# Optimization experiments

Hardware: AMD Instinct MI355X
Metric: run time of the kernel (lower is better)

Reference implementation:

```python
import jax, jax.numpy as jnp
import numpy as np

THETA = 10000.0

def apply_rope(x, positions):
    # x: [B, H, S, d_k], positions: [S] int
    d_k = x.shape[-1]
    inv_freq = THETA ** (-jnp.arange(0, d_k, 2, dtype=jnp.float32) / d_k)  # [d_k/2]
    ang = positions.astype(jnp.float32)[:, None] * inv_freq[None, :]        # [S, d_k/2]
    cos, sin = jnp.cos(ang), jnp.sin(ang)
    x_even = x[..., 0::2]
    x_odd = x[..., 1::2]
    r_even = x_even * cos - x_odd * sin
    r_odd = x_even * sin + x_odd * cos
    # interleave back
    return jnp.stack([r_even, r_odd], axis=-1).reshape(x.shape)

def setup_inputs() -> dict:
    key = jax.random.key(0)
    k1, k2, k3 = jax.random.split(key, 3)
    B, S, D = 2, 2048, 1024
    x = jax.random.normal(k1, (B, S, D), dtype=jnp.float32)
    token_positions = jnp.arange(S, dtype=jnp.int32)
    W_qkv = jax.random.normal(k2, (3 * D, D), dtype=jnp.float32) * 0.02
    W_o = jax.random.normal(k3, (D, D), dtype=jnp.float32) * 0.02
    return {"x": x, "token_positions": token_positions, "W_qkv": W_qkv, "W_o": W_o}

def reference(x, token_positions, W_qkv, W_o):
    B, S, D = x.shape
    H = 16
    d_k = D // H
    qkv = jnp.einsum('bsd,ed->bse', x, W_qkv)           # [B, S, 3D]
    q, k, v = jnp.split(qkv, 3, axis=-1)
    def to_heads(t):
        return t.reshape(B, S, H, d_k).transpose(0, 2, 1, 3)  # [B, H, S, d_k]
    hq, hk, hv = to_heads(q), to_heads(k), to_heads(v)
    hq = apply_rope(hq, token_positions)
    hk = apply_rope(hk, token_positions)
    scale = d_k ** -0.5
    scores = jnp.einsum('bhqd,bhkd->bhqk', hq, hk) * scale  # [B, H, S, S]
    causal = jnp.tril(jnp.ones((S, S), dtype=bool))
    scores = jnp.where(causal, scores, -jnp.inf)
    attn = jax.nn.softmax(scores, axis=-1)
    out = jnp.einsum('bhqk,bhkd->bhqd', attn, hv)           # [B, H, S, d_k]
    out = out.transpose(0, 2, 1, 3).reshape(B, S, D)
    return jnp.einsum('bsd,ed->bse', out, W_o)
```

## Files before the change

### kernel.cpp

```cpp
#include <hip/hip_runtime.h>
#include <math.h>

typedef short short8 __attribute__((ext_vector_type(8)));
typedef float f32x4 __attribute__((ext_vector_type(4)));

typedef __attribute__((address_space(1))) const void* as1p;
typedef __attribute__((address_space(3))) void* as3p;

__device__ __forceinline__ unsigned short f2bf(float f) {
    unsigned int u = __float_as_uint(f);
    u += 0x7fffu + ((u >> 16) & 1u);
    return (unsigned short)(u >> 16);
}
__device__ __forceinline__ float bf2f(unsigned int bits) {
    return __uint_as_float(bits << 16);
}

__global__ void cvt_all_bf16(const float* __restrict__ x,
                             const float* __restrict__ wqkv,
                             const float* __restrict__ wo,
                             unsigned short* __restrict__ xb,
                             unsigned short* __restrict__ wqkvb,
                             unsigned short* __restrict__ wob) {
    int i = blockIdx.x * blockDim.x + threadIdx.x;
    const float* src;
    unsigned short* dst;
    int off;
    if (i < 1048576)       { src = x;    dst = xb;    off = i; }
    else if (i < 1835008)  { src = wqkv; dst = wqkvb; off = i - 1048576; }
    else                   { src = wo;   dst = wob;   off = i - 1835008; }
    float4 v = ((const float4*)src)[off];
    ushort4 o = make_ushort4(f2bf(v.x), f2bf(v.y), f2bf(v.z), f2bf(v.w));
    ((ushort4*)dst)[off] = o;
}

template <int RF, int NTX, bool BF16_OUT, bool DO_ROPE>
__global__ __launch_bounds__(256) void gemm_nt_mfma(
    const unsigned short* __restrict__ A, const unsigned short* __restrict__ B,
    void* __restrict__ Cv, const int* __restrict__ pos, int N, int K) {
    constexpr int BM = RF * 32;
    __shared__ unsigned short As[BM * 32];
    __shared__ unsigned short Bs[128 * 32];
    const int tid = threadIdx.x;
    const int wave = tid >> 6, lane = tid & 63;
    const int L = blockIdx.x;
    const int xcd = L & 7, idx = L >> 3;
    const int nt_ = xcd * NTX + idx % NTX;
    const int mt  = idx / NTX;
    const int m0 = mt * BM, n0 = nt_ << 7;
    const int wr = ((wave >> 1) & 1) * (RF * 16);
    const int wc = (wave & 1) << 6;

    const int r0 = tid >> 2, ko = (tid & 3) << 3;
    const unsigned short* Ap0 = A + (size_t)(m0 + r0) * K + ko;
    const unsigned short* Ap1 = A + (size_t)(m0 + (RF == 4 ? 64 : 0) + r0) * K + ko;
    const unsigned short* Bp0 = B + (size_t)(n0 + r0) * K + ko;
    const unsigned short* Bp1 = B + (size_t)(n0 + 64 + r0) * K + ko;

    f32x4 acc[RF][4] = {};
    const int lro = lane & 15, g8 = (lane >> 4) << 3;

    for (int k0 = 0; k0 < K; k0 += 32) {
        __syncthreads();
        __builtin_amdgcn_global_load_lds((as1p)(Ap0 + k0), (as3p)(As + tid * 8), 16, 0, 0);
        if constexpr (RF == 4)
            __builtin_amdgcn_global_load_lds((as1p)(Ap1 + k0), (as3p)(As + (256 + tid) * 8), 16, 0, 0);
        __builtin_amdgcn_global_load_lds((as1p)(Bp0 + k0), (as3p)(Bs + tid * 8), 16, 0, 0);
        __builtin_amdgcn_global_load_lds((as1p)(Bp1 + k0), (as3p)(Bs + (256 + tid) * 8), 16, 0, 0);
        __syncthreads();

        short8 af[RF], bfr[4];
        #pragma unroll
        for (int i = 0; i < RF; i++) af[i] = *(const short8*)&As[(wr + i * 16 + lro) * 32 + g8];
        #pragma unroll
        for (int j = 0; j < 4; j++) bfr[j] = *(const short8*)&Bs[(wc + j * 16 + lro) * 32 + g8];
        #pragma unroll
        for (int i = 0; i < RF; i++)
            #pragma unroll
            for (int j = 0; j < 4; j++)
                acc[i][j] = __builtin_amdgcn_mfma_f32_16x16x32_bf16(af[i], bfr[j], acc[i][j], 0, 0, 0);
    }

    const int row_b = m0 + wr + ((lane >> 4) << 2);
    const int col_b = n0 + wc + lro;

    if constexpr (DO_ROPE) {
        const int sec = (n0 + wc) >> 10;
        if (sec < 2) {
            const float qs = (sec == 0) ? 0.18033688011112042f : 1.0f;
            const float sgn = (lane & 1) ? 1.0f : -1.0f;
            float ps[RF * 4];
            #pragma unroll
            for (int i = 0; i < RF; i++)
                #pragma unroll
                for (int r = 0; r < 4; r++)
                    ps[i * 4 + r] = (float)pos[(row_b + i * 16 + r) & 2047];
            #pragma unroll
            for (int j = 0; j < 4; j++) {
                float invf_rev = exp2f(-(float)((lro >> 1) + 8 * j) * 0.41524101186092029f)
                                 * 0.15915494309189535f;
                #pragma unroll
                for (int i = 0; i < RF; i++)
                    #pragma unroll
                    for (int r = 0; r < 4; r++) {
                        float rev = ps[i * 4 + r] * invf_rev;
                        rev -= floorf(rev);
                        float c = __builtin_amdgcn_cosf(rev) * qs;
                        float s = __builtin_amdgcn_sinf(rev) * (qs * sgn);
                        float mine = acc[i][j][r];
                        float partner = __shfl_xor(mine, 1, 64);
                        acc[i][j][r] = mine * c + partner * s;
                    }
            }
        }
    }

    #pragma unroll
    for (int i = 0; i < RF; i++)
        #pragma unroll
        for (int j = 0; j < 4; j++)
            #pragma unroll
            for (int r = 0; r < 4; r++) {
                size_t idx2 = (size_t)(row_b + i * 16 + r) * N + (col_b + j * 16);
                if constexpr (BF16_OUT) ((unsigned short*)Cv)[idx2] = f2bf(acc[i][j][r]);
                else ((float*)Cv)[idx2] = acc[i][j][r];
            }
}

__global__ __launch_bounds__(256) void flash_attn_mfma(
    const unsigned short* __restrict__ qkv, unsigned short* __restrict__ Ows) {
    const int S = 2048, D3 = 3072;
    const int L = blockIdx.x;
    const int xcd = L & 7, t = L >> 3;
    const int g2 = xcd + ((t >> 5) << 3);
    const int h = g2 & 15, b = g2 >> 4;
    const int qt = 31 - (t & 31);
    const int q0 = qt << 6, nkt = qt + 1;
    const int tid = threadIdx.x, wave = tid >> 6, lane = tid & 63;
    const int lro = lane & 15, grp = lane >> 4;

    __shared__ __align__(16) unsigned short Ks[2][64 * 64];
    __shared__ __align__(16) unsigned int   Vp[2][64 * 36];
    __shared__ __align__(16) unsigned short Ps[64 * 80];

    const int sr = tid >> 3;
    const int sc = ((tid & 7) ^ (sr & 7)) << 3;
    const int kp = tid >> 3, vo = (tid & 7) << 3;
    const int vka = (kp >> 1) + ((kp & 1) << 5);
    const int vcol = (((kp >> 2) ^ (tid & 7)) << 2) | (kp & 3);

    const int cq = grp ^ (lro & 7);
    int kof0[4], kof1[4], vbse[4], vq[4];
    #pragma unroll
    for (int nt = 0; nt < 4; nt++) {
        int R = nt * 16 + lro;
        kof0[nt] = R * 64 + cq * 8;
        kof1[nt] = R * 64 + (cq ^ 4) * 8;
        vbse[nt] = R * 36;
        vq[nt] = (grp ^ (R >> 3)) << 2;
    }
    const int apo = (wave * 16 + lro) * 80 + grp * 8;
    const int prow = wave * 16 + grp * 4;

    const unsigned short* kbg = qkv + (size_t)(b * S) * D3 + 1024 + h * 64;
    const unsigned short* vbg = qkv + (size_t)(b * S) * D3 + 2048 + h * 64;

    const unsigned short* qrow =
        qkv + (size_t)(b * S + q0 + wave * 16 + lro) * D3 + h * 64 + grp * 8;
    short8 aq0 = *(const short8*)qrow;
    short8 aq1 = *(const short8*)(qrow + 32);

    __builtin_amdgcn_global_load_lds((as1p)(kbg + (size_t)sr * D3 + sc),
                                     (as3p)&Ks[0][tid * 8], 16, 0, 0);
    __builtin_amdgcn_global_load_lds((as1p)(kbg + (size_t)(sr + 32) * D3 + sc),
                                     (as3p)&Ks[0][(tid + 256) * 8], 16, 0, 0);
    {
        const unsigned short* vs = vbg + (size_t)vka * D3 + vo;
        uint4 va = *(const uint4*)vs;
        uint4 vb = *(const uint4*)(vs + (size_t)16 * D3);
        const unsigned short* pa = (const unsigned short*)&va;
        const unsigned short* pb = (const unsigned short*)&vb;
        #pragma unroll
        for (int j = 0; j < 8; j++)
            Vp[0][(vo + j) * 36 + vcol] = (unsigned)pa[j] | ((unsigned)pb[j] << 16);
    }
    __syncthreads();

    f32x4 acc_o[4] = {};
    float lsum[4] = {0.f, 0.f, 0.f, 0.f};

    for (int kt = 0; kt < nkt; kt++) {
        const int cur = kt & 1, nxt = cur ^ 1;
        const bool pf = (kt + 1 < nkt);
        uint4 va, vb;
        if (pf) {
            const unsigned short* kb1 = kbg + (size_t)((kt + 1) * 64) * D3;
            __builtin_amdgcn_global_load_lds((as1p)(kb1 + (size_t)sr * D3 + sc),
                                             (as3p)&Ks[nxt][tid * 8], 16, 0, 0);
            __builtin_amdgcn_global_load_lds((as1p)(kb1 + (size_t)(sr + 32) * D3 + sc),
                                             (as3p)&Ks[nxt][(tid + 256) * 8], 16, 0, 0);
            const unsigned short* vs = vbg + (size_t)((kt + 1) * 64 + vka) * D3 + vo;
            va = *(const uint4*)vs;
            vb = *(const uint4*)(vs + (size_t)16 * D3);
        }

        f32x4 s[4] = {};
        #pragma unroll
        for (int nt = 0; nt < 4; nt++) {
            short8 bk0 = *(const short8*)&Ks[cur][kof0[nt]];
            short8 bk1 = *(const short8*)&Ks[cur][kof1[nt]];
            s[nt] = __builtin_amdgcn_mfma_f32_16x16x32_bf16(aq0, bk0, s[nt], 0, 0, 0);
            s[nt] = __builtin_amdgcn_mfma_f32_16x16x32_bf16(aq1, bk1, s[nt], 0, 0, 0);
        }

        const bool diag = (kt == nkt - 1);
        #pragma unroll
        for (int r = 0; r < 4; r++) {
            float v0 = s[0][r], v1 = s[1][r], v2 = s[2][r], v3 = s[3][r];
            if (diag) {
                int rowl = prow + r;
                if (lro > rowl) v0 = -1e30f;
                if (16 + lro > rowl) v1 = -1e30f;
                if (32 + lro > rowl) v2 = -1e30f;
                if (48 + lro > rowl) v3 = -1e30f;
            }
            float p0 = __builtin_amdgcn_exp2f(v0);
            float p1 = __builtin_amdgcn_exp2f(v1);
            float p2 = __builtin_amdgcn_exp2f(v2);
            float p3 = __builtin_amdgcn_exp2f(v3);
            lsum[r] += (p0 + p1) + (p2 + p3);
            unsigned u0 = __float_as_uint(p0) + 0x8000u;
            unsigned u1 = __float_as_uint(p1) + 0x8000u;
            unsigned u2 = __float_as_uint(p2) + 0x8000u;
            unsigned u3 = __float_as_uint(p3) + 0x8000u;
            uint2 w = make_uint2((u0 >> 16) | (u1 & 0xffff0000u),
                                 (u2 >> 16) | (u3 & 0xffff0000u));
            *(uint2*)&Ps[(prow + r) * 80 + lro * 4] = w;
        }

        short8 ap0 = *(const short8*)&Ps[apo];
        short8 ap1 = *(const short8*)&Ps[apo + 32];
        #pragma unroll
        for (int nt = 0; nt < 4; nt++) {
            short8 bv0 = *(const short8*)&Vp[cur][vbse[nt] + vq[nt]];
            short8 bv1 = *(const short8*)&Vp[cur][vbse[nt] + (vq[nt] ^ 16)];
            acc_o[nt] = __builtin_amdgcn_mfma_f32_16x16x32_bf16(ap0, bv0, acc_o[nt], 0, 0, 0);
            acc_o[nt] = __builtin_amdgcn_mfma_f32_16x16x32_bf16(ap1, bv1, acc_o[nt], 0, 0, 0);
        }

        if (pf) {
            const unsigned short* pa = (const unsigned short*)&va;
            const unsigned short* pb = (const unsigned short*)&vb;
            #pragma unroll
            for (int j = 0; j < 8; j++)
                Vp[nxt][(vo + j) * 36 + vcol] = (unsigned)pa[j] | ((unsigned)pb[j] << 16);
        }
        __syncthreads();
    }

    #pragma unroll
    for (int r = 0; r < 4; r++) {
        float rsum = lsum[r];
        #pragma unroll
        for (int off = 1; off < 16; off <<= 1)
            rsum += __shfl_xor(rsum, off, 16);
        float inv = 1.0f / rsum;
        int row = q0 + prow + r;
        #pragma unroll
        for (int nt = 0; nt < 4; nt++)
            Ows[(size_t)(b * S + row) * 1024 + h * 64 + nt * 16 + lro] =
                f2bf(acc_o[nt][r] * inv);
    }
}

extern "C" void kernel_launch(void* const* d_in, const int* in_sizes, int n_in,
                              void* d_out, int out_size, void* d_ws, size_t ws_size,
                              hipStream_t stream) {
    const float* x    = (const float*)d_in[0];
    const int*   pos  = (const int*)d_in[1];
    const float* Wqkv = (const float*)d_in[2];
    const float* Wo   = (const float*)d_in[3];
    float* out = (float*)d_out;

    unsigned short* xb    = (unsigned short*)d_ws;
    unsigned short* Wqkvb = xb + (size_t)4096 * 1024;
    unsigned short* Wob   = Wqkvb + (size_t)3072 * 1024;
    unsigned short* qkvb  = Wob + (size_t)1024 * 1024;
    unsigned short* Owsb  = qkvb + (size_t)4096 * 3072;

    cvt_all_bf16<<<8192, 256, 0, stream>>>(x, Wqkv, Wo, xb, Wqkvb, Wob);

    gemm_nt_mfma<4, 3, true, true><<<768, 256, 0, stream>>>(
        xb, Wqkvb, qkvb, pos, 3072, 1024);

    flash_attn_mfma<<<1024, 256, 0, stream>>>(qkvb, Owsb);

    gemm_nt_mfma<2, 1, false, false><<<512, 256, 0, stream>>>(
        Owsb, Wob, out, nullptr, 1024, 1024);
}
```

Before: 201.2 us.

## Double-buffer GEMM LDS tiles and pair causal query tiles per attention block

```diff
diff --git a/kernel.cpp b/kernel.cpp
--- a/kernel.cpp
+++ b/kernel.cpp
@@ -39,8 +39,8 @@
     const unsigned short* __restrict__ A, const unsigned short* __restrict__ B,
     void* __restrict__ Cv, const int* __restrict__ pos, int N, int K) {
     constexpr int BM = RF * 32;
-    __shared__ unsigned short As[BM * 32];
-    __shared__ unsigned short Bs[128 * 32];
+    __shared__ unsigned short As[2][BM * 32];
+    __shared__ unsigned short Bs[2][128 * 32];
     const int tid = threadIdx.x;
     const int wave = tid >> 6, lane = tid & 63;
     const int L = blockIdx.x;
@@ -60,25 +60,38 @@
     f32x4 acc[RF][4] = {};
     const int lro = lane & 15, g8 = (lane >> 4) << 3;
 
+    __builtin_amdgcn_global_load_lds((as1p)Ap0, (as3p)(As[0] + tid * 8), 16, 0, 0);
+    if constexpr (RF == 4)
+        __builtin_amdgcn_global_load_lds((as1p)Ap1, (as3p)(As[0] + (256 + tid) * 8), 16, 0, 0);
+    __builtin_amdgcn_global_load_lds((as1p)Bp0, (as3p)(Bs[0] + tid * 8), 16, 0, 0);
+    __builtin_amdgcn_global_load_lds((as1p)Bp1, (as3p)(Bs[0] + (256 + tid) * 8), 16, 0, 0);
+    __syncthreads();
+
     for (int k0 = 0; k0 < K; k0 += 32) {
-        __syncthreads();
-        __builtin_amdgcn_global_load_lds((as1p)(Ap0 + k0), (as3p)(As + tid * 8), 16, 0, 0);
-        if constexpr (RF == 4)
-            __builtin_amdgcn_global_load_lds((as1p)(Ap1 + k0), (as3p)(As + (256 + tid) * 8), 16, 0, 0);
-        __builtin_amdgcn_global_load_lds((as1p)(Bp0 + k0), (as3p)(Bs + tid * 8), 16, 0, 0);
-        __builtin_amdgcn_global_load_lds((as1p)(Bp1 + k0), (as3p)(Bs + (256 + tid) * 8), 16, 0, 0);
-        __syncthreads();
+        const int cur = (k0 >> 5) & 1, nxt = cur ^ 1;
+        if (k0 + 32 < K) {
+            __builtin_amdgcn_global_load_lds((as1p)(Ap0 + k0 + 32),
+                                             (as3p)(As[nxt] + tid * 8), 16, 0, 0);
+            if constexpr (RF == 4)
+                __builtin_amdgcn_global_load_lds((as1p)(Ap1 + k0 + 32),
+                                                 (as3p)(As[nxt] + (256 + tid) * 8), 16, 0, 0);
+            __builtin_amdgcn_global_load_lds((as1p)(Bp0 + k0 + 32),
+                                             (as3p)(Bs[nxt] + tid * 8), 16, 0, 0);
+            __builtin_amdgcn_global_load_lds((as1p)(Bp1 + k0 + 32),
+                                             (as3p)(Bs[nxt] + (256 + tid) * 8), 16, 0, 0);
+        }
 
         short8 af[RF], bfr[4];
         #pragma unroll
-        for (int i = 0; i < RF; i++) af[i] = *(const short8*)&As[(wr + i * 16 + lro) * 32 + g8];
-        #pragma unroll
-        for (int j = 0; j < 4; j++) bfr[j] = *(const short8*)&Bs[(wc + j * 16 + lro) * 32 + g8];
+        for (int i = 0; i < RF; i++) af[i] = *(const short8*)&As[cur][(wr + i * 16 + lro) * 32 + g8];
+        #pragma unroll
+        for (int j = 0; j < 4; j++) bfr[j] = *(const short8*)&Bs[cur][(wc + j * 16 + lro) * 32 + g8];
         #pragma unroll
         for (int i = 0; i < RF; i++)
             #pragma unroll
             for (int j = 0; j < 4; j++)
                 acc[i][j] = __builtin_amdgcn_mfma_f32_16x16x32_bf16(af[i], bfr[j], acc[i][j], 0, 0, 0);
+        __syncthreads();
     }
 
     const int row_b = m0 + wr + ((lane >> 4) << 2);
@@ -130,12 +143,11 @@
 __global__ __launch_bounds__(256) void flash_attn_mfma(
     const unsigned short* __restrict__ qkv, unsigned short* __restrict__ Ows) {
     const int S = 2048, D3 = 3072;
-    const int L = blockIdx.x;
+    const int L = blockIdx.x + (blockIdx.y << 4) + (blockIdx.z << 8);
     const int xcd = L & 7, t = L >> 3;
-    const int g2 = xcd + ((t >> 5) << 3);
+    const int pp = t & 15;
+    const int g2 = xcd + ((t >> 4) << 3);
     const int h = g2 & 15, b = g2 >> 4;
-    const int qt = 31 - (t & 31);
-    const int q0 = qt << 6, nkt = qt + 1;
     const int tid = threadIdx.x, wave = tid >> 6, lane = tid & 63;
     const int lro = lane & 15, grp = lane >> 4;
 
@@ -165,111 +177,118 @@
     const unsigned short* kbg = qkv + (size_t)(b * S) * D3 + 1024 + h * 64;
     const unsigned short* vbg = qkv + (size_t)(b * S) * D3 + 2048 + h * 64;
 
-    const unsigned short* qrow =
-        qkv + (size_t)(b * S + q0 + wave * 16 + lro) * D3 + h * 64 + grp * 8;
-    short8 aq0 = *(const short8*)qrow;
-    short8 aq1 = *(const short8*)(qrow + 32);
-
-    __builtin_amdgcn_global_load_lds((as1p)(kbg + (size_t)sr * D3 + sc),
-                                     (as3p)&Ks[0][tid * 8], 16, 0, 0);
-    __builtin_amdgcn_global_load_lds((as1p)(kbg + (size_t)(sr + 32) * D3 + sc),
-                                     (as3p)&Ks[0][(tid + 256) * 8], 16, 0, 0);
-    {
-        const unsigned short* vs = vbg + (size_t)vka * D3 + vo;
-        uint4 va = *(const uint4*)vs;
-        uint4 vb = *(const uint4*)(vs + (size_t)16 * D3);
-        const unsigned short* pa = (const unsigned short*)&va;
-        const unsigned short* pb = (const unsigned short*)&vb;
-        #pragma unroll
-        for (int j = 0; j < 8; j++)
-            Vp[0][(vo + j) * 36 + vcol] = (unsigned)pa[j] | ((unsigned)pb[j] << 16);
-    }
-    __syncthreads();
-
-    f32x4 acc_o[4] = {};
-    float lsum[4] = {0.f, 0.f, 0.f, 0.f};
-
-    for (int kt = 0; kt < nkt; kt++) {
-        const int cur = kt & 1, nxt = cur ^ 1;
-        const bool pf = (kt + 1 < nkt);
-        uint4 va, vb;
-        if (pf) {
-            const unsigned short* kb1 = kbg + (size_t)((kt + 1) * 64) * D3;
-            __builtin_amdgcn_global_load_lds((as1p)(kb1 + (size_t)sr * D3 + sc),
-                                             (as3p)&Ks[nxt][tid * 8], 16, 0, 0);
-            __builtin_amdgcn_global_load_lds((as1p)(kb1 + (size_t)(sr + 32) * D3 + sc),
-                                             (as3p)&Ks[nxt][(tid + 256) * 8], 16, 0, 0);
-            const unsigned short* vs = vbg + (size_t)((kt + 1) * 64 + vka) * D3 + vo;
-            va = *(const uint4*)vs;
-            vb = *(const uint4*)(vs + (size_t)16 * D3);
-        }
-
-        f32x4 s[4] = {};
-        #pragma unroll
-        for (int nt = 0; nt < 4; nt++) {
-            short8 bk0 = *(const short8*)&Ks[cur][kof0[nt]];
-            short8 bk1 = *(const short8*)&Ks[cur][kof1[nt]];
-            s[nt] = __builtin_amdgcn_mfma_f32_16x16x32_bf16(aq0, bk0, s[nt], 0, 0, 0);
-            s[nt] = __builtin_amdgcn_mfma_f32_16x16x32_bf16(aq1, bk1, s[nt], 0, 0, 0);
-        }
-
-        const bool diag = (kt == nkt - 1);
-        #pragma unroll
-        for (int r = 0; r < 4; r++) {
-            float v0 = s[0][r], v1 = s[1][r], v2 = s[2][r], v3 = s[3][r];
-            if (diag) {
-                int rowl = prow + r;
-                if (lro > rowl) v0 = -1e30f;
-                if (16 + lro > rowl) v1 = -1e30f;
-                if (32 + lro > rowl) v2 = -1e30f;
-                if (48 + lro > rowl) v3 = -1e30f;
-            }
-            float p0 = __builtin_amdgcn_exp2f(v0);
-            float p1 = __builtin_amdgcn_exp2f(v1);
-            float p2 = __builtin_amdgcn_exp2f(v2);
-            float p3 = __builtin_amdgcn_exp2f(v3);
-            lsum[r] += (p0 + p1) + (p2 + p3);
-            unsigned u0 = __float_as_uint(p0) + 0x8000u;
-            unsigned u1 = __float_as_uint(p1) + 0x8000u;
-            unsigned u2 = __float_as_uint(p2) + 0x8000u;
-            unsigned u3 = __float_as_uint(p3) + 0x8000u;
-            uint2 w = make_uint2((u0 >> 16) | (u1 & 0xffff0000u),
-                                 (u2 >> 16) | (u3 & 0xffff0000u));
-            *(uint2*)&Ps[(prow + r) * 80 + lro * 4] = w;
-        }
-
-        short8 ap0 = *(const short8*)&Ps[apo];
-        short8 ap1 = *(const short8*)&Ps[apo + 32];
-        #pragma unroll
-        for (int nt = 0; nt < 4; nt++) {
-            short8 bv0 = *(const short8*)&Vp[cur][vbse[nt] + vq[nt]];
-            short8 bv1 = *(const short8*)&Vp[cur][vbse[nt] + (vq[nt] ^ 16)];
-            acc_o[nt] = __builtin_amdgcn_mfma_f32_16x16x32_bf16(ap0, bv0, acc_o[nt], 0, 0, 0);
-            acc_o[nt] = __builtin_amdgcn_mfma_f32_16x16x32_bf16(ap1, bv1, acc_o[nt], 0, 0, 0);
-        }
-
-        if (pf) {
+    for (int ph = 0; ph < 2; ph++) {
+        const int qt = ph ? 31 - pp : pp;
+        const int q0 = qt << 6;
+        const int nkt = qt + 1;
+
+        __syncthreads();
+        const unsigned short* qrow =
+            qkv + (size_t)(b * S + q0 + wave * 16 + lro) * D3 + h * 64 + grp * 8;
+        short8 aq0 = *(const short8*)qrow;
+        short8 aq1 = *(const short8*)(qrow + 32);
+
+        __builtin_amdgcn_global_load_lds((as1p)(kbg + (size_t)sr * D3 + sc),
+                                         (as3p)&Ks[0][tid * 8], 16, 0, 0);
+        __builtin_amdgcn_global_load_lds((as1p)(kbg + (size_t)(sr + 32) * D3 + sc),
+                                         (as3p)&Ks[0][(tid + 256) * 8], 16, 0, 0);
+        {
+            const unsigned short* vs = vbg + (size_t)vka * D3 + vo;
+            uint4 va = *(const uint4*)vs;
+            uint4 vb = *(const uint4*)(vs + (size_t)16 * D3);
             const unsigned short* pa = (const unsigned short*)&va;
             const unsigned short* pb = (const unsigned short*)&vb;
             #pragma unroll
             for (int j = 0; j < 8; j++)
-                Vp[nxt][(vo + j) * 36 + vcol] = (unsigned)pa[j] | ((unsigned)pb[j] << 16);
+                Vp[0][(vo + j) * 36 + vcol] = (unsigned)pa[j] | ((unsigned)pb[j] << 16);
         }
         __syncthreads();
-    }
-
-    #pragma unroll
-    for (int r = 0; r < 4; r++) {
-        float rsum = lsum[r];
-        #pragma unroll
-        for (int off = 1; off < 16; off <<= 1)
-            rsum += __shfl_xor(rsum, off, 16);
-        float inv = 1.0f / rsum;
-        int row = q0 + prow + r;
-        #pragma unroll
-        for (int nt = 0; nt < 4; nt++)
-            Ows[(size_t)(b * S + row) * 1024 + h * 64 + nt * 16 + lro] =
-                f2bf(acc_o[nt][r] * inv);
+
+        f32x4 acc_o[4] = {};
+        float lsum[4] = {0.f, 0.f, 0.f, 0.f};
+
+        for (int kt = 0; kt < nkt; kt++) {
+            const int cur = kt & 1, nxt = cur ^ 1;
+            const bool pf = (kt + 1 < nkt);
+            uint4 va, vb;
+            if (pf) {
+                const unsigned short* kb1 = kbg + (size_t)((kt + 1) * 64) * D3;
+                __builtin_amdgcn_global_load_lds((as1p)(kb1 + (size_t)sr * D3 + sc),
+                                                 (as3p)&Ks[nxt][tid * 8], 16, 0, 0);
+                __builtin_amdgcn_global_load_lds((as1p)(kb1 + (size_t)(sr + 32) * D3 + sc),
+                                                 (as3p)&Ks[nxt][(tid + 256) * 8], 16, 0, 0);
+                const unsigned short* vs = vbg + (size_t)((kt + 1) * 64 + vka) * D3 + vo;
+                va = *(const uint4*)vs;
+                vb = *(const uint4*)(vs + (size_t)16 * D3);
+            }
+
+            f32x4 s[4] = {};
+            #pragma unroll
+            for (int nt = 0; nt < 4; nt++) {
+                short8 bk0 = *(const short8*)&Ks[cur][kof0[nt]];
+                short8 bk1 = *(const short8*)&Ks[cur][kof1[nt]];
+                s[nt] = __builtin_amdgcn_mfma_f32_16x16x32_bf16(aq0, bk0, s[nt], 0, 0, 0);
+                s[nt] = __builtin_amdgcn_mfma_f32_16x16x32_bf16(aq1, bk1, s[nt], 0, 0, 0);
+            }
+
+            const bool diag = (kt == nkt - 1);
+            #pragma unroll
+            for (int r = 0; r < 4; r++) {
+                float v0 = s[0][r], v1 = s[1][r], v2 = s[2][r], v3 = s[3][r];
+                if (diag) {
+                    int rowl = prow + r;
+                    if (lro > rowl) v0 = -1e30f;
+                    if (16 + lro > rowl) v1 = -1e30f;
+                    if (32 + lro > rowl) v2 = -1e30f;
+                    if (48 + lro > rowl) v3 = -1e30f;
+                }
+                float p0 = __builtin_amdgcn_exp2f(v0);
+                float p1 = __builtin_amdgcn_exp2f(v1);
+                float p2 = __builtin_amdgcn_exp2f(v2);
+                float p3 = __builtin_amdgcn_exp2f(v3);
+                lsum[r] += (p0 + p1) + (p2 + p3);
+                unsigned u0 = __float_as_uint(p0) + 0x8000u;
+                unsigned u1 = __float_as_uint(p1) + 0x8000u;
+                unsigned u2 = __float_as_uint(p2) + 0x8000u;
+                unsigned u3 = __float_as_uint(p3) + 0x8000u;
+                uint2 w = make_uint2((u0 >> 16) | (u1 & 0xffff0000u),
+                                     (u2 >> 16) | (u3 & 0xffff0000u));
+                *(uint2*)&Ps[(prow + r) * 80 + lro * 4] = w;
+            }
+
+            short8 ap0 = *(const short8*)&Ps[apo];
+            short8 ap1 = *(const short8*)&Ps[apo + 32];
+            #pragma unroll
+            for (int nt = 0; nt < 4; nt++) {
+                short8 bv0 = *(const short8*)&Vp[cur][vbse[nt] + vq[nt]];
+                short8 bv1 = *(const short8*)&Vp[cur][vbse[nt] + (vq[nt] ^ 16)];
+                acc_o[nt] = __builtin_amdgcn_mfma_f32_16x16x32_bf16(ap0, bv0, acc_o[nt], 0, 0, 0);
+                acc_o[nt] = __builtin_amdgcn_mfma_f32_16x16x32_bf16(ap1, bv1, acc_o[nt], 0, 0, 0);
+            }
+
+            if (pf) {
+                const unsigned short* pa = (const unsigned short*)&va;
+                const unsigned short* pb = (const unsigned short*)&vb;
+                #pragma unroll
+                for (int j = 0; j < 8; j++)
+                    Vp[nxt][(vo + j) * 36 + vcol] = (unsigned)pa[j] | ((unsigned)pb[j] << 16);
+            }
+            __syncthreads();
+        }
+
+        #pragma unroll
+        for (int r = 0; r < 4; r++) {
+            float rsum = lsum[r];
+            #pragma unroll
+            for (int off = 1; off < 16; off <<= 1)
+                rsum += __shfl_xor(rsum, off, 16);
+            float inv = 1.0f / rsum;
+            int row = q0 + prow + r;
+            #pragma unroll
+            for (int nt = 0; nt < 4; nt++)
+                Ows[(size_t)(b * S + row) * 1024 + h * 64 + nt * 16 + lro] =
+                    f2bf(acc_o[nt][r] * inv);
+        }
     }
 }
 
@@ -293,7 +312,7 @@
     gemm_nt_mfma<4, 3, true, true><<<768, 256, 0, stream>>>(
         xb, Wqkvb, qkvb, pos, 3072, 1024);
 
-    flash_attn_mfma<<<1024, 256, 0, stream>>>(qkvb, Owsb);
+    flash_attn_mfma<<<dim3(16, 16, 2), 256, 0, stream>>>(qkvb, Owsb);
 
     gemm_nt_mfma<2, 1, false, false><<<512, 256, 0, stream>>>(
         Owsb, Wob, out, nullptr, 1024, 1024);
```

After: 196.0 us. 2.6% less time.
